# Kernel optimization log

Hardware: AMD Instinct MI355X
Metric: run time of the kernel (lower is better)

The kernel has to match this reference:

```python
import jax, jax.numpy as jnp
import numpy as np

# (in_ch, out_ch) per conv layer per SA stage (use_xyz adds +3 to first in-ch)
DIMS = {1: [(3, 64), (64, 64), (64, 128)],
        2: [(131, 128), (128, 128), (128, 256)],
        3: [(259, 256), (256, 512), (512, 1024)]}
B, N = 32, 4096


def setup_inputs() -> dict:
    key = jax.random.key(0)
    key, k = jax.random.split(key)
    inp = {"pointcloud": jax.random.uniform(k, (B, N, 3), jnp.float32)}
    for s in (1, 2, 3):
        for l, (ci, co) in enumerate(DIMS[s]):
            key, k1, k2, k3 = jax.random.split(key, 4)
            inp[f"w{s}{l}"] = jax.random.normal(k1, (ci, co), jnp.float32) * (1.0 / np.sqrt(ci))
            # eval-mode BatchNorm folded to per-channel scale g and bias b
            inp[f"g{s}{l}"] = 1.0 + 0.1 * jax.random.normal(k2, (co,), jnp.float32)
            inp[f"b{s}{l}"] = 0.1 * jax.random.normal(k3, (co,), jnp.float32)
    return inp


def fps(xyz, npoint):
    """Farthest point sampling. xyz: (B,N,3) -> idx (B,npoint) int32. First index is 0."""
    n = xyz.shape[1]
    def one(pts):
        def body(carry, _):
            dist, last = carry
            d = jnp.sum((pts - pts[last]) ** 2, axis=-1)
            dist = jnp.minimum(dist, d)
            nxt = jnp.argmax(dist).astype(jnp.int32)
            return (dist, nxt), nxt
        init = (jnp.full((n,), 1e10, pts.dtype), jnp.int32(0))
        _, idxs = jax.lax.scan(body, init, None, length=npoint - 1)
        return jnp.concatenate([jnp.zeros((1,), jnp.int32), idxs])
    return jax.vmap(one)(xyz)


def ball_query(xyz, centers, radius, nsample):
    """xyz (B,N,3), centers (B,S,3) -> idx (B,S,nsample): first nsample in-ball point
    indices, deficits padded with the first found index (matches CUDA ball_query)."""
    n = xyz.shape[1]
    d2 = jnp.sum((centers[:, :, None, :] - xyz[:, None, :, :]) ** 2, axis=-1)  # (B,S,N)
    keyv = jnp.where(d2 < radius * radius, jnp.arange(n)[None, None, :], n)
    sk = jnp.sort(keyv, axis=-1)[..., :nsample]  # ascending valid indices, pad = n
    first = sk[..., :1]
    idx = jnp.where(sk == n, first, sk)
    return jnp.clip(idx, 0, n - 1)


def gather(pts, idx):
    """pts (B,N,C), idx (B,...) -> (B,...,C)"""
    return jax.vmap(lambda p, i: p[i])(pts, idx)


def shared_mlp(x, params):
    """x (..., Cin); each layer: 1x1 conv (matmul) + folded-BN affine + ReLU."""
    for w, g, b in params:
        x = jax.nn.relu(jnp.einsum('...c,cd->...d', x, w) * g + b)
    return x


def sa_module(xyz, feat, npoint, radius, nsample, params):
    ctr_idx = fps(xyz, npoint)
    new_xyz = gather(xyz, ctr_idx)                        # (B,S,3)
    idx = ball_query(xyz, new_xyz, radius, nsample)       # (B,S,K)
    g_xyz = gather(xyz, idx) - new_xyz[:, :, None, :]     # (B,S,K,3) centered
    grouped = g_xyz if feat is None else jnp.concatenate([g_xyz, gather(feat, idx)], axis=-1)
    h = shared_mlp(grouped, params)                       # (B,S,K,Cout)
    return new_xyz, jnp.max(h, axis=2)                    # max-pool over neighbors


def reference(pointcloud, w10, g10, b10, w11, g11, b11, w12, g12, b12,
              w20, g20, b20, w21, g21, b21, w22, g22, b22,
              w30, g30, b30, w31, g31, b31, w32, g32, b32):
    p1 = [(w10, g10, b10), (w11, g11, b11), (w12, g12, b12)]
    p2 = [(w20, g20, b20), (w21, g21, b21), (w22, g22, b22)]
    p3 = [(w30, g30, b30), (w31, g31, b31), (w32, g32, b32)]
    xyz = pointcloud[..., :3]
    xyz, feat = sa_module(xyz, None, 512, 0.2, 64, p1)
    xyz, feat = sa_module(xyz, feat, 128, 0.4, 64, p2)
    # group-all SA: one group containing all points, xyz NOT centered
    grouped = jnp.concatenate([xyz, feat], axis=-1)[:, None]  # (B,1,S,259)
    h = shared_mlp(grouped, p3)                                # (B,1,S,1024)
    return jnp.max(h, axis=2)[:, 0]                            # (B,1024)
```

## Files before the change

### kernel.cpp

```cpp
#include <hip/hip_runtime.h>
#include <math.h>

#define NTH 256

using short8 = __attribute__((ext_vector_type(8))) short;
using f32x4  = __attribute__((ext_vector_type(4))) float;

__device__ __forceinline__ unsigned short f2bf(float x) {
    unsigned u = __float_as_uint(x);
    u += 0x7fff + ((u >> 16) & 1);
    return (unsigned short)(u >> 16);
}
__device__ __forceinline__ float bf2f(unsigned short h) {
    return __uint_as_float(((unsigned)h) << 16);
}

template<int CTRL>
__device__ __forceinline__ unsigned long long dppmax(unsigned long long k) {
    unsigned lo = (unsigned)k, hi = (unsigned)(k >> 32);
    unsigned plo = (unsigned)__builtin_amdgcn_update_dpp(0, (int)lo, CTRL, 0xF, 0xF, true);
    unsigned phi = (unsigned)__builtin_amdgcn_update_dpp(0, (int)hi, CTRL, 0xF, 0xF, true);
    unsigned long long p = ((unsigned long long)phi << 32) | plo;
    return p > k ? p : k;
}

template<int N, int NPOINT, int NTHR, int NPC, bool INIT, bool SPILL>
__device__ __forceinline__ void fps_body(
    const float* __restrict__ xyz, float* __restrict__ out_xyz, int b, int it0,
    float* __restrict__ pts , float* __restrict__ ctr ,
    unsigned long long* __restrict__ wkey ,
    float* __restrict__ sdist, int* __restrict__ slast)
{
    constexpr int PT = N / NTHR;
    constexpr int NW = NTHR / 64;
    const int tid  = threadIdx.x;
    const int lane = tid & 63;
    const int w    = tid >> 6;
    const float* src = xyz + (size_t)b * N * 3;

    __builtin_amdgcn_s_setprio(1);

    for (int e = tid; e < N * 3; e += NTHR) pts[e] = src[e];

    float px[PT], py[PT], pz[PT], dist[PT];
    unsigned klo[PT];
#pragma unroll
    for (int j = 0; j < PT; ++j) {
        int i = j * NTHR + tid;
        px[j] = src[i * 3 + 0]; py[j] = src[i * 3 + 1]; pz[j] = src[i * 3 + 2];
        klo[j] = ~(unsigned)i;
        dist[j] = 1e10f;
    }
    int last = 0;
    if constexpr (!INIT) {
        const float* sd = sdist + (size_t)b * N;
#pragma unroll
        for (int j = 0; j < PT; ++j) dist[j] = sd[j * NTHR + tid];
        last = slast[b];
    } else {
        if (tid == 0) { ctr[0] = src[0]; ctr[1] = src[1]; ctr[2] = src[2]; }
    }
    __syncthreads();

    constexpr int CBEG = INIT ? 1 : 0;
    for (int c = CBEG; c < NPC; ++c) {
        const float lx = pts[last * 3 + 0];
        const float ly = pts[last * 3 + 1];
        const float lz = pts[last * 3 + 2];
        unsigned long long best = 0ull;
#pragma unroll
        for (int j = 0; j < PT; ++j) {
            float dx = px[j] - lx, dy = py[j] - ly, dz = pz[j] - lz;
            float d = __fadd_rn(__fadd_rn(__fmul_rn(dx, dx), __fmul_rn(dy, dy)),
                                __fmul_rn(dz, dz));
            float nd = fminf(dist[j], d);
            dist[j] = nd;
            unsigned long long key =
                ((unsigned long long)__float_as_uint(nd) << 32) | (unsigned long long)klo[j];
            best = (key > best) ? key : best;
        }
        best = dppmax<0xB1>(best);
        best = dppmax<0x4E>(best);
        best = dppmax<0x141>(best);
        best = dppmax<0x140>(best);
        best = dppmax<0x142>(best);
        best = dppmax<0x143>(best);
        const int p = (c & 1) * NW;
        if (lane == 63) wkey[p + w] = best;
        __syncthreads();
        unsigned long long K0[NW];
#pragma unroll
        for (int v = 0; v < NW; ++v) K0[v] = wkey[p + v];
#pragma unroll
        for (int st = NW / 2; st > 0; st >>= 1)
#pragma unroll
            for (int v = 0; v < st; ++v) K0[v] = (K0[v + st] > K0[v]) ? K0[v + st] : K0[v];
        last = (int)(~(unsigned)K0[0]);
        if (tid == 0) {
            ctr[c * 3 + 0] = pts[last * 3 + 0];
            ctr[c * 3 + 1] = pts[last * 3 + 1];
            ctr[c * 3 + 2] = pts[last * 3 + 2];
        }
    }
    __syncthreads();
    if constexpr (SPILL) {
        float* sd = sdist + (size_t)b * N;
#pragma unroll
        for (int j = 0; j < PT; ++j) sd[j * NTHR + tid] = dist[j];
        if (tid == 0) slast[b] = last;
    }
    float* dst = out_xyz + ((size_t)b * NPOINT + (it0 - CBEG)) * 3;
    for (int e = tid; e < NPC * 3; e += NTHR) dst[e] = ctr[e];
    __builtin_amdgcn_s_setprio(0);
}

#define PREP_TOT 813056
__device__ __forceinline__ void prep_body(
    int gid, int stride,
    const float* __restrict__ w0, const float* __restrict__ w1, const float* __restrict__ w2,
    const float* __restrict__ w3, const float* __restrict__ w4, const float* __restrict__ w5,
    const float* __restrict__ w6, const float* __restrict__ w7, const float* __restrict__ w8,
    unsigned short* __restrict__ outw)
{
    const int K_[9]    = {3, 64, 64, 131, 128, 128, 259, 256, 512};
    const int N_[9]    = {64, 64, 128, 128, 128, 256, 256, 512, 1024};
    const int E_[9]    = {2048, 4096, 8192, 20480, 16384, 32768, 73728, 131072, 524288};
    const int base_[9] = {0, 4096, 12288, 28672, 69632, 102400, 167936, 315392, 577536};
    const int PCF_[9]  = {0, 0, 0, 128, 0, 0, 256, 0, 0};
    const float* W_[9] = {w0, w1, w2, w3, w4, w5, w6, w7, w8};
    for (; gid < PREP_TOT; gid += stride) {
        int i = 0, t = gid;
        while (t >= E_[i]) { t -= E_[i]; ++i; }
        const int Nn = N_[i];
        const int k8 = t / (Nn * 8);
        const int rem = t - k8 * Nn * 8;
        const int col = rem >> 3, j = rem & 7;
        const int k = k8 * 8 + j;
        float v = 0.f;
        if (k < K_[i]) {
            int ks = k;
            const int pcf = PCF_[i];
            if (pcf > 0) ks = (k < pcf) ? (k + 3) : (k - pcf);
            v = W_[i][(size_t)ks * Nn + col];
        }
        unsigned short hi = f2bf(v);
        unsigned short lo = f2bf(v - bf2f(hi));
        outw[base_[i] + t] = hi;
        outw[base_[i] + E_[i] + t] = lo;
    }
}

template<int K, int NSUB, int NOFF, int NFULL, int RTILES, int SX, int SY, bool FINAL>
__device__ __forceinline__ void mfma_layer(
    const unsigned short* __restrict__ whi, const unsigned short* __restrict__ wlo,
    const float* __restrict__ gm, const float* __restrict__ bt,
    const unsigned short* __restrict__ Xhi, const unsigned short* __restrict__ Xlo,
    unsigned short* __restrict__ Yhi, unsigned short* __restrict__ Ylo,
    float* outp, int tid)
{
    constexpr int KP  = (K + 31) & ~31;
    constexpr int KC  = KP / 32;
    constexpr int NTW = NSUB / 64;
    static_assert(NSUB % 64 == 0, "col split");
    const int w = tid >> 6, lane = tid & 63;
    const int lr = lane & 15, lg = lane >> 4;
    const int colbase = NOFF + w * (NSUB / 4);

    f32x4 acc[RTILES][NTW];
#pragma unroll
    for (int m = 0; m < RTILES; ++m)
#pragma unroll
        for (int t = 0; t < NTW; ++t) acc[m][t] = f32x4{0.f, 0.f, 0.f, 0.f};

    const unsigned short* xh0 = Xhi + lr * SX + lg * 8;
    const unsigned short* xl0 = Xlo + lr * SX + lg * 8;

    for (int kc = 0; kc < KC; ++kc) {
        const size_t krow = (size_t)(kc * 4 + lg) * NFULL * 8;
        short8 bh[NTW], bl[NTW];
#pragma unroll
        for (int t = 0; t < NTW; ++t) {
            const int col = colbase + t * 16 + lr;
            bh[t] = *reinterpret_cast<const short8*>(whi + krow + (size_t)col * 8);
            bl[t] = *reinterpret_cast<const short8*>(wlo + krow + (size_t)col * 8);
        }
#pragma unroll
        for (int m = 0; m < RTILES; ++m) {
            short8 ah = *reinterpret_cast<const short8*>(xh0 + m * 16 * SX + kc * 32);
            short8 al = *reinterpret_cast<const short8*>(xl0 + m * 16 * SX + kc * 32);
#pragma unroll
            for (int t = 0; t < NTW; ++t) {
                acc[m][t] = __builtin_amdgcn_mfma_f32_16x16x32_bf16(ah, bh[t], acc[m][t], 0, 0, 0);
                acc[m][t] = __builtin_amdgcn_mfma_f32_16x16x32_bf16(ah, bl[t], acc[m][t], 0, 0, 0);
                acc[m][t] = __builtin_amdgcn_mfma_f32_16x16x32_bf16(al, bh[t], acc[m][t], 0, 0, 0);
            }
        }
    }
#pragma unroll
    for (int t = 0; t < NTW; ++t) {
        const int col = colbase + t * 16 + lr;
        const float gv = gm[col], bv = bt[col];
        if constexpr (FINAL) {
            float mx = 0.f;
#pragma unroll
            for (int m = 0; m < RTILES; ++m)
#pragma unroll
                for (int r = 0; r < 4; ++r)
                    mx = fmaxf(mx, fmaxf(fmaf(acc[m][t][r], gv, bv), 0.f));
            mx = fmaxf(mx, __shfl_xor(mx, 16));
            mx = fmaxf(mx, __shfl_xor(mx, 32));
            if (lg == 0)
                atomicMax(reinterpret_cast<int*>(outp) + col, __float_as_int(mx));
        } else {
#pragma unroll
            for (int m = 0; m < RTILES; ++m)
#pragma unroll
                for (int r = 0; r < 4; ++r) {
                    float v = fmaxf(fmaf(acc[m][t][r], gv, bv), 0.f);
                    unsigned short hi = f2bf(v);
                    unsigned short lo = f2bf(v - bf2f(hi));
                    const int row = m * 16 + lg * 4 + r;
                    Yhi[row * SY + col] = hi;
                    Ylo[row * SY + col] = lo;
                }
        }
    }
}

template<int CF, int C0, int C1, int C2, int R>
struct SaCfg {
    static constexpr int CIN = 3 + CF;
    static constexpr int KP0 = (CIN + 31) & ~31;
    static constexpr int SX = KP0 + 8, SY1 = C0 + 8, SY2 = C1 + 8;
    static constexpr int RT = R / 16;
    static constexpr int OFF_Y1 = 0;
    static constexpr int OFF_X = 2 * R * SY1;
    static constexpr int XSZ = 2 * R * SX, Y2SZ = 2 * R * SY2;
    static constexpr int TOT = OFF_X + (XSZ > Y2SZ ? XSZ : Y2SZ);
    static constexpr int BYTES = TOT * 2 + 264 * 4;
};

template<int CF, int C0, int C1, int C2, int R>
__device__ __forceinline__ void sa_body(
    unsigned short* __restrict__ sm, int* __restrict__ bqm,
    int b, int cs, int S, int half,
    const float* __restrict__ src_xyz, const float* __restrict__ src_feat,
    const float* __restrict__ centers,
    const unsigned short* __restrict__ w0h, const unsigned short* __restrict__ w0l,
    const unsigned short* __restrict__ w1h, const unsigned short* __restrict__ w1l,
    const unsigned short* __restrict__ w2h, const unsigned short* __restrict__ w2l,
    const float* __restrict__ g0, const float* __restrict__ b0,
    const float* __restrict__ g1, const float* __restrict__ b1,
    const float* __restrict__ g2, const float* __restrict__ b2,
    float* __restrict__ out_feat, int N, float r2)
{
    using C = SaCfg<CF, C0, C1, C2, R>;
    constexpr int TPR = NTH / R;
    const int tid  = threadIdx.x;
    const int lane = tid & 63;
    const int w    = tid >> 6;
    const int bs   = b * S + cs;

    const float cx = centers[(size_t)bs * 3 + 0];
    const float cy = centers[(size_t)bs * 3 + 1];
    const float cz = centers[(size_t)bs * 3 + 2];

    {
        const int seg = N >> 2;
        const float* px = src_xyz + (size_t)b * N * 3;
        int count = 0, first = -1;
        const int bend = (w + 1) * seg;
        for (int base = w * seg; base < bend && count < 64; base += 64) {
            int i = base + lane;
            float dx = px[i * 3 + 0] - cx, dy = px[i * 3 + 1] - cy, dz = px[i * 3 + 2] - cz;
            float d2 = __fadd_rn(__fadd_rn(__fmul_rn(dx, dx), __fmul_rn(dy, dy)),
                                 __fmul_rn(dz, dz));
            bool inb = d2 < r2;
            unsigned long long m = __ballot(inb);
            if (first < 0 && m) first = base + (__ffsll(m) - 1);
            if (inb) {
                int pos = count + (int)__popcll(m & ((1ull << lane) - 1ull));
                if (pos < 64) bqm[w * 64 + pos] = i;
            }
            count += (int)__popcll(m);
        }
        if (lane == 0) {
            bqm[256 + w] = count > 64 ? 64 : count;
            bqm[260 + w] = first;
        }
    }
    __syncthreads();

    unsigned short* Xhi = sm + C::OFF_X;    unsigned short* Xlo = Xhi + R * C::SX;
    unsigned short* Y1h = sm + C::OFF_Y1;   unsigned short* Y1l = Y1h + R * C::SY1;
    unsigned short* Y2h = sm + C::OFF_X;    unsigned short* Y2l = Y2h + R * C::SY2;

    {
        const int r = tid / TPR, s = tid % TPR;
        int pid;
        {
            const int cA = bqm[256 + 0], cB = bqm[256 + 1], cC = bqm[256 + 2], cD = bqm[256 + 3];
            const int tot = cA + cB + cC + cD;
            int t = half * R + r;
            if (t < tot) {
                int ww = 0;
                if (t >= cA) { t -= cA; ww = 1;
                    if (t >= cB) { t -= cB; ww = 2;
                        if (t >= cC) { t -= cC; ww = 3; } } }
                pid = bqm[ww * 64 + t];
            } else {
                const int fA = bqm[260 + 0], fB = bqm[260 + 1], fC = bqm[260 + 2], fD = bqm[260 + 3];
                pid = fA >= 0 ? fA : (fB >= 0 ? fB : (fC >= 0 ? fC : (fD >= 0 ? fD : (N - 1))));
            }
        }
        unsigned short* xh = Xhi + r * C::SX;
        unsigned short* xl = Xlo + r * C::SX;
        if constexpr (CF > 0) {
            constexpr int CPT = CF / TPR;
            const float* frow = src_feat + ((size_t)b * N + pid) * CF + s * CPT;
#pragma unroll
            for (int q = 0; q < CPT / 4; ++q) {
                float4 v4 = *reinterpret_cast<const float4*>(frow + q * 4);
                ushort4 h, l;
                h.x = f2bf(v4.x); l.x = f2bf(v4.x - bf2f(h.x));
                h.y = f2bf(v4.y); l.y = f2bf(v4.y - bf2f(h.y));
                h.z = f2bf(v4.z); l.z = f2bf(v4.z - bf2f(h.z));
                h.w = f2bf(v4.w); l.w = f2bf(v4.w - bf2f(h.w));
                *reinterpret_cast<ushort4*>(xh + s * CPT + q * 4) = h;
                *reinterpret_cast<ushort4*>(xl + s * CPT + q * 4) = l;
            }
        }
        if (s < 3) {
            float p = src_xyz[((size_t)b * N + pid) * 3 + s]
                      - (s == 0 ? cx : (s == 1 ? cy : cz));
            unsigned short hi = f2bf(p), lo = f2bf(p - bf2f(hi));
            xh[CF + s] = hi; xl[CF + s] = lo;
        }
        constexpr int PADPER = (C::KP0 - C::CIN + TPR - 1) / TPR;
#pragma unroll
        for (int q = 0; q < PADPER; ++q) {
            int c = C::CIN + s * PADPER + q;
            if (c < C::KP0) { xh[c] = 0; xl[c] = 0; }
        }
    }
    __syncthreads();
    mfma_layer<C::CIN, C0, 0, C0, C::RT, C::SX, C::SY1, false>(
        w0h, w0l, g0, b0, Xhi, Xlo, Y1h, Y1l, nullptr, tid);
    __syncthreads();
    mfma_layer<C0, C1, 0, C1, C::RT, C::SY1, C::SY2, false>(
        w1h, w1l, g1, b1, Y1h, Y1l, Y2h, Y2l, nullptr, tid);
    __syncthreads();
    mfma_layer<C1, C2, 0, C2, C::RT, C::SY2, 0, true>(
        w2h, w2l, g2, b2, Y2h, Y2l, nullptr, nullptr,
        out_feat + (size_t)bs * C2, tid);
}

template<int N1>
__global__ __launch_bounds__(NTH) void k_fps1a_prep(
    const float* __restrict__ pc, float* __restrict__ nxyz1,
    const float* __restrict__ w0, const float* __restrict__ w1, const float* __restrict__ w2,
    const float* __restrict__ w3, const float* __restrict__ w4, const float* __restrict__ w5,
    const float* __restrict__ w6, const float* __restrict__ w7, const float* __restrict__ w8,
    unsigned short* __restrict__ outw,
    float* __restrict__ sdist, int* __restrict__ slast, int nfps)
{
    __shared__ float pts[N1 * 3];
    __shared__ float ctr[256 * 3];
    __shared__ unsigned long long wkey[2 * (NTH / 64)];
    if ((int)blockIdx.x < nfps) {
        fps_body<N1, 512, NTH, 256, true, true>(pc, nxyz1, blockIdx.x, 1,
                                                pts, ctr, wkey, sdist, slast);
    } else {
        prep_body((blockIdx.x - nfps) * NTH + threadIdx.x,
                  (gridDim.x - nfps) * NTH,
                  w0, w1, w2, w3, w4, w5, w6, w7, w8, outw);
    }
}

__global__ __launch_bounds__(NTH) void k_fps1b_sa1h1(
    const float* __restrict__ pc, float* __restrict__ nxyz1,
    float* __restrict__ sdist, int* __restrict__ slast,
    const unsigned short* __restrict__ w0h, const unsigned short* __restrict__ w0l,
    const unsigned short* __restrict__ w1h, const unsigned short* __restrict__ w1l,
    const unsigned short* __restrict__ w2h, const unsigned short* __restrict__ w2l,
    const float* __restrict__ g0, const float* __restrict__ b0,
    const float* __restrict__ g1, const float* __restrict__ b1,
    const float* __restrict__ g2, const float* __restrict__ b2,
    float* __restrict__ feat1, float r2)
{
    constexpr int FPSB = 4096 * 3 * 4 + 256 * 3 * 4 + 2 * (NTH / 64) * 8;
    constexpr int SAB  = SaCfg<0, 64, 64, 128, 64>::BYTES;
    constexpr int BYTES = FPSB > SAB ? FPSB : SAB;
    __shared__ __align__(16) char raw[BYTES];
    if ((int)blockIdx.x < 32) {
        float* pts = (float*)raw;
        float* ctr = (float*)(raw + 4096 * 3 * 4);
        unsigned long long* wkey = (unsigned long long*)(raw + 4096 * 3 * 4 + 256 * 3 * 4);
        fps_body<4096, 512, NTH, 256, false, false>(pc, nxyz1, blockIdx.x, 256,
                                                    pts, ctr, wkey, sdist, slast);
    } else {
        const int blk = blockIdx.x - 32;
        const int b = blk >> 8, cs = blk & 255;
        unsigned short* sm = (unsigned short*)raw;
        int* bqm = (int*)(raw + SaCfg<0, 64, 64, 128, 64>::TOT * 2);
        sa_body<0, 64, 64, 128, 64>(sm, bqm, b, cs, 512, 0,
                                    pc, nullptr, nxyz1,
                                    w0h, w0l, w1h, w1l, w2h, w2l,
                                    g0, b0, g1, b1, g2, b2, feat1, 4096, r2);
    }
}

__global__ __launch_bounds__(NTH) void k_fps2_sa1h2(
    const float* __restrict__ pc, const float* __restrict__ nxyz1_c,
    float* __restrict__ nxyz1, float* __restrict__ nxyz2,
    const unsigned short* __restrict__ w0h, const unsigned short* __restrict__ w0l,
    const unsigned short* __restrict__ w1h, const unsigned short* __restrict__ w1l,
    const unsigned short* __restrict__ w2h, const unsigned short* __restrict__ w2l,
    const float* __restrict__ g0, const float* __restrict__ b0,
    const float* __restrict__ g1, const float* __restrict__ b1,
    const float* __restrict__ g2, const float* __restrict__ b2,
    float* __restrict__ feat1, float r2)
{
    constexpr int FPSB = 512 * 3 * 4 + 128 * 3 * 4 + 2 * (NTH / 64) * 8;
    constexpr int SAB  = SaCfg<0, 64, 64, 128, 64>::BYTES;
    constexpr int BYTES = FPSB > SAB ? FPSB : SAB;
    __shared__ __align__(16) char raw[BYTES];
    if ((int)blockIdx.x < 32) {
        float* pts = (float*)raw;
        float* ctr = (float*)(raw + 512 * 3 * 4);
        unsigned long long* wkey = (unsigned long long*)(raw + 512 * 3 * 4 + 128 * 3 * 4);
        fps_body<512, 128, NTH, 128, true, false>(nxyz1, nxyz2, blockIdx.x, 1,
                                                  pts, ctr, wkey, nullptr, nullptr);
    } else {
        const int blk = blockIdx.x - 32;
        const int b = blk >> 8, cs = 256 + (blk & 255);
        unsigned short* sm = (unsigned short*)raw;
        int* bqm = (int*)(raw + SaCfg<0, 64, 64, 128, 64>::TOT * 2);
        sa_body<0, 64, 64, 128, 64>(sm, bqm, b, cs, 512, 0,
                                    pc, nullptr, nxyz1_c,
                                    w0h, w0l, w1h, w1l, w2h, w2l,
                                    g0, b0, g1, b1, g2, b2, feat1, 4096, r2);
    }
}

__global__ __launch_bounds__(NTH) void k_sa2(
    const float* __restrict__ nxyz1, const float* __restrict__ feat1,
    const float* __restrict__ nxyz2,
    const unsigned short* __restrict__ w0h, const unsigned short* __restrict__ w0l,
    const unsigned short* __restrict__ w1h, const unsigned short* __restrict__ w1l,
    const unsigned short* __restrict__ w2h, const unsigned short* __restrict__ w2l,
    const float* __restrict__ g0, const float* __restrict__ b0,
    const float* __restrict__ g1, const float* __restrict__ b1,
    const float* __restrict__ g2, const float* __restrict__ b2,
    float* __restrict__ feat2, float r2)
{
    using C = SaCfg<128, 128, 128, 256, 32>;
    __shared__ __align__(16) char raw[C::BYTES];
    const int half = blockIdx.x & 1;
    const int cb   = blockIdx.x >> 1;
    const int b = cb >> 7, cs = cb & 127;
    unsigned short* sm = (unsigned short*)raw;
    int* bqm = (int*)(raw + C::TOT * 2);
    sa_body<128, 128, 128, 256, 32>(sm, bqm, b, cs, 128, half,
                                    nxyz1, feat1, nxyz2,
                                    w0h, w0l, w1h, w1l, w2h, w2l,
                                    g0, b0, g1, b1, g2, b2, feat2, 512, r2);
}

template<int CF, int C0, int C1, int C2>
__global__ __launch_bounds__(NTH) void head_mfma(
    const float* __restrict__ xyz, const float* __restrict__ feat,
    const unsigned short* __restrict__ w0h, const unsigned short* __restrict__ w0l,
    const unsigned short* __restrict__ w1h, const unsigned short* __restrict__ w1l,
    const unsigned short* __restrict__ w2h, const unsigned short* __restrict__ w2l,
    const float* __restrict__ g0, const float* __restrict__ b0,
    const float* __restrict__ g1, const float* __restrict__ b1,
    const float* __restrict__ g2, const float* __restrict__ b2,
    float* __restrict__ out, int Np)
{
    constexpr int R = 16;
    constexpr int CIN = 3 + CF;
    constexpr int KP0 = (CIN + 31) & ~31;
    constexpr int SX = KP0 + 8, SY1 = C0 + 8, SY2 = C1 + 8;
    constexpr int OFF_Y1 = 0;
    constexpr int OFF_X  = 2 * R * SY1;
    constexpr int XSZ = 2 * R * SX, Y2SZ = 2 * R * SY2;
    constexpr int TOT = OFF_X + (XSZ > Y2SZ ? XSZ : Y2SZ);
    __shared__ __align__(16) unsigned short sm[TOT];
    constexpr int TPR = NTH / R;

    const int tid = threadIdx.x;
    const int chunks = Np / R;
    const int b  = blockIdx.x / chunks;
    const int r0 = (blockIdx.x % chunks) * R;

    unsigned short* Xhi = sm + OFF_X;   unsigned short* Xlo = Xhi + R * SX;
    unsigned short* Y1h = sm + OFF_Y1;  unsigned short* Y1l = Y1h + R * SY1;
    unsigned short* Y2h = sm + OFF_X;   unsigned short* Y2l = Y2h + R * SY2;

    {
        const int r = tid / TPR, s = tid % TPR;
        const int row = r0 + r;
        unsigned short* xh = Xhi + r * SX;
        unsigned short* xl = Xlo + r * SX;
        constexpr int CPT = CF / TPR;
        const float* frow = feat + ((size_t)b * Np + row) * CF + s * CPT;
#pragma unroll
        for (int q = 0; q < CPT / 4; ++q) {
            float4 v4 = *reinterpret_cast<const float4*>(frow + q * 4);
            ushort4 h, l;
            h.x = f2bf(v4.x); l.x = f2bf(v4.x - bf2f(h.x));
            h.y = f2bf(v4.y); l.y = f2bf(v4.y - bf2f(h.y));
            h.z = f2bf(v4.z); l.z = f2bf(v4.z - bf2f(h.z));
            h.w = f2bf(v4.w); l.w = f2bf(v4.w - bf2f(h.w));
            *reinterpret_cast<ushort4*>(xh + s * CPT + q * 4) = h;
            *reinterpret_cast<ushort4*>(xl + s * CPT + q * 4) = l;
        }
        if (s < 3) {
            float p = xyz[((size_t)b * Np + row) * 3 + s];
            unsigned short hi = f2bf(p), lo = f2bf(p - bf2f(hi));
            xh[CF + s] = hi; xl[CF + s] = lo;
        }
        constexpr int PADPER = (KP0 - CIN + TPR - 1) / TPR;
#pragma unroll
        for (int q = 0; q < PADPER; ++q) {
            int c = CIN + s * PADPER + q;
            if (c < KP0) { xh[c] = 0; xl[c] = 0; }
        }
    }
    __syncthreads();
    mfma_layer<CIN, C0, 0, C0, 1, SX, SY1, false>(w0h, w0l, g0, b0, Xhi, Xlo, Y1h, Y1l, nullptr, tid);
    __syncthreads();
    mfma_layer<C0, C1, 0, C1, 1, SY1, SY2, false>(w1h, w1l, g1, b1, Y1h, Y1l, Y2h, Y2l, nullptr, tid);
    __syncthreads();
    float* op = out + (size_t)b * C2;
    mfma_layer<C1, C2 / 2, 0,      C2, 1, SY2, 0, true>(w2h, w2l, g2, b2, Y2h, Y2l, nullptr, nullptr, op, tid);
    mfma_layer<C1, C2 / 2, C2 / 2, C2, 1, SY2, 0, true>(w2h, w2l, g2, b2, Y2h, Y2l, nullptr, nullptr, op, tid);
}

extern "C" void kernel_launch(void* const* d_in, const int* in_sizes, int n_in,
                              void* d_out, int out_size, void* d_ws, size_t ws_size,
                              hipStream_t stream)
{
    (void)in_sizes; (void)n_in; (void)ws_size;
    const int B = 32;
    const float* pc = (const float*)d_in[0];
    const float* W[27];
    for (int i = 0; i < 27; ++i) W[i] = (const float*)d_in[1 + i];
    float* out = (float*)d_out;

    char* ws = (char*)d_ws;
    size_t off = 0;
    auto take = [&](size_t bytes) {
        void* p = ws + off;
        off += (bytes + 255) & ~(size_t)255;
        return p;
    };
    float* nxyz1 = (float*)take((size_t)B * 512 * 3 * 4);
    float* feat1 = (float*)take((size_t)B * 512 * 128 * 4);
    float* nxyz2 = (float*)take((size_t)B * 128 * 3 * 4);
    float* feat2 = (float*)take((size_t)B * 128 * 256 * 4);
    unsigned short* wf = (unsigned short*)take((size_t)1626112 * 2);
    float* sdist = (float*)take((size_t)B * 4096 * 4);
    int*   slast = (int*)take((size_t)B * 4);

    const int E_[9]    = {2048, 4096, 8192, 20480, 16384, 32768, 73728, 131072, 524288};
    const int base_[9] = {0, 4096, 12288, 28672, 69632, 102400, 167936, 315392, 577536};
    const unsigned short* wh[9]; const unsigned short* wl[9];
    for (int i = 0; i < 9; ++i) { wh[i] = wf + base_[i]; wl[i] = wf + base_[i] + E_[i]; }

    hipMemsetAsync(feat1, 0, (size_t)B * 512 * 128 * 4, stream);
    hipMemsetAsync(feat2, 0, (size_t)B * 128 * 256 * 4, stream);
    hipMemsetAsync(d_out, 0, (size_t)out_size * 4, stream);

    const float r2_1 = (float)(0.2 * 0.2);
    const float r2_2 = (float)(0.4 * 0.4);

    k_fps1a_prep<4096><<<32 + 512, NTH, 0, stream>>>(
        pc, nxyz1,
        W[0], W[3], W[6], W[9], W[12], W[15], W[18], W[21], W[24],
        wf, sdist, slast, 32);

    k_fps1b_sa1h1<<<32 + B * 256, NTH, 0, stream>>>(
        pc, nxyz1, sdist, slast,
        wh[0], wl[0], wh[1], wl[1], wh[2], wl[2],
        W[1], W[2], W[4], W[5], W[7], W[8],
        feat1, r2_1);

    k_fps2_sa1h2<<<32 + B * 256, NTH, 0, stream>>>(
        pc, nxyz1, nxyz1, nxyz2,
        wh[0], wl[0], wh[1], wl[1], wh[2], wl[2],
        W[1], W[2], W[4], W[5], W[7], W[8],
        feat1, r2_1);

    k_sa2<<<B * 128 * 2, NTH, 0, stream>>>(
        nxyz1, feat1, nxyz2,
        wh[3], wl[3], wh[4], wl[4], wh[5], wl[5],
        W[10], W[11], W[13], W[14], W[16], W[17],
        feat2, r2_2);

    head_mfma<256, 256, 512, 1024><<<B * 8, NTH, 0, stream>>>(
        nxyz2, feat2,
        wh[6], wl[6], wh[7], wl[7], wh[8], wl[8],
        W[19], W[20], W[22], W[23], W[25], W[26],
        out, 128);
}
```

Before: 612.4 us.

## Fold output zeroing into prep kernel and run stage-2 FPS after stage-1 FPS

Three hipMemsetAsync calls are replaced by zeroing blocks appended to the first prep/FPS kernel, which removes separate memset launches. The second-stage FPS now runs inside the same blocks that finish the first-stage FPS, right after it completes. The second SA1 half is therefore a plain SA kernel. This shortens the serial FPS chain across kernel boundaries, but stage-2 FPS now overlaps with the SA1 first-half blocks instead of the second-half ones.

```diff
diff --git a/kernel.cpp b/kernel.cpp
--- a/kernel.cpp
+++ b/kernel.cpp
@@ -362,7 +362,9 @@
     const float* __restrict__ w3, const float* __restrict__ w4, const float* __restrict__ w5,
     const float* __restrict__ w6, const float* __restrict__ w7, const float* __restrict__ w8,
     unsigned short* __restrict__ outw,
-    float* __restrict__ sdist, int* __restrict__ slast, int nfps)
+    float* __restrict__ sdist, int* __restrict__ slast,
+    float4* __restrict__ z1, int n1, float4* __restrict__ z2, int n2,
+    float4* __restrict__ z3, int n3, int nfps, int nprep)
 {
     __shared__ float pts[N1 * 3];
     __shared__ float ctr[256 * 3];
@@ -370,15 +372,21 @@
     if ((int)blockIdx.x < nfps) {
         fps_body<N1, 512, NTH, 256, true, true>(pc, nxyz1, blockIdx.x, 1,
                                                 pts, ctr, wkey, sdist, slast);
+    } else if ((int)blockIdx.x < nfps + nprep) {
+        prep_body((blockIdx.x - nfps) * NTH + threadIdx.x, nprep * NTH,
+                  w0, w1, w2, w3, w4, w5, w6, w7, w8, outw);
     } else {
-        prep_body((blockIdx.x - nfps) * NTH + threadIdx.x,
-                  (gridDim.x - nfps) * NTH,
-                  w0, w1, w2, w3, w4, w5, w6, w7, w8, outw);
-    }
-}
-
-__global__ __launch_bounds__(NTH) void k_fps1b_sa1h1(
-    const float* __restrict__ pc, float* __restrict__ nxyz1,
+        const int zid = (blockIdx.x - nfps - nprep) * NTH + threadIdx.x;
+        const int zs  = (gridDim.x - nfps - nprep) * NTH;
+        const float4 zv = make_float4(0.f, 0.f, 0.f, 0.f);
+        for (int i = zid; i < n1; i += zs) z1[i] = zv;
+        for (int i = zid; i < n2; i += zs) z2[i] = zv;
+        for (int i = zid; i < n3; i += zs) z3[i] = zv;
+    }
+}
+
+__global__ __launch_bounds__(NTH) void k_fps1b2_sa1h1(
+    const float* __restrict__ pc, float* __restrict__ nxyz1, float* __restrict__ nxyz2,
     float* __restrict__ sdist, int* __restrict__ slast,
     const unsigned short* __restrict__ w0h, const unsigned short* __restrict__ w0l,
     const unsigned short* __restrict__ w1h, const unsigned short* __restrict__ w1l,
@@ -393,11 +401,21 @@
     constexpr int BYTES = FPSB > SAB ? FPSB : SAB;
     __shared__ __align__(16) char raw[BYTES];
     if ((int)blockIdx.x < 32) {
-        float* pts = (float*)raw;
-        float* ctr = (float*)(raw + 4096 * 3 * 4);
-        unsigned long long* wkey = (unsigned long long*)(raw + 4096 * 3 * 4 + 256 * 3 * 4);
-        fps_body<4096, 512, NTH, 256, false, false>(pc, nxyz1, blockIdx.x, 256,
-                                                    pts, ctr, wkey, sdist, slast);
+        {
+            float* pts = (float*)raw;
+            float* ctr = (float*)(raw + 4096 * 3 * 4);
+            unsigned long long* wkey = (unsigned long long*)(raw + 4096 * 3 * 4 + 256 * 3 * 4);
+            fps_body<4096, 512, NTH, 256, false, false>(pc, nxyz1, blockIdx.x, 256,
+                                                        pts, ctr, wkey, sdist, slast);
+        }
+        __syncthreads();
+        {
+            float* pts = (float*)raw;
+            float* ctr = (float*)(raw + 512 * 3 * 4);
+            unsigned long long* wkey = (unsigned long long*)(raw + 512 * 3 * 4 + 128 * 3 * 4);
+            fps_body<512, 128, NTH, 128, true, false>(nxyz1, nxyz2, blockIdx.x, 1,
+                                                      pts, ctr, wkey, nullptr, nullptr);
+        }
     } else {
         const int blk = blockIdx.x - 32;
         const int b = blk >> 8, cs = blk & 255;
@@ -410,9 +428,8 @@
     }
 }
 
-__global__ __launch_bounds__(NTH) void k_fps2_sa1h2(
-    const float* __restrict__ pc, const float* __restrict__ nxyz1_c,
-    float* __restrict__ nxyz1, float* __restrict__ nxyz2,
+__global__ __launch_bounds__(NTH) void k_sa1h2(
+    const float* __restrict__ pc, const float* __restrict__ nxyz1,
     const unsigned short* __restrict__ w0h, const unsigned short* __restrict__ w0l,
     const unsigned short* __restrict__ w1h, const unsigned short* __restrict__ w1l,
     const unsigned short* __restrict__ w2h, const unsigned short* __restrict__ w2l,
@@ -421,26 +438,15 @@
     const float* __restrict__ g2, const float* __restrict__ b2,
     float* __restrict__ feat1, float r2)
 {
-    constexpr int FPSB = 512 * 3 * 4 + 128 * 3 * 4 + 2 * (NTH / 64) * 8;
-    constexpr int SAB  = SaCfg<0, 64, 64, 128, 64>::BYTES;
-    constexpr int BYTES = FPSB > SAB ? FPSB : SAB;
-    __shared__ __align__(16) char raw[BYTES];
-    if ((int)blockIdx.x < 32) {
-        float* pts = (float*)raw;
-        float* ctr = (float*)(raw + 512 * 3 * 4);
-        unsigned long long* wkey = (unsigned long long*)(raw + 512 * 3 * 4 + 128 * 3 * 4);
-        fps_body<512, 128, NTH, 128, true, false>(nxyz1, nxyz2, blockIdx.x, 1,
-                                                  pts, ctr, wkey, nullptr, nullptr);
-    } else {
-        const int blk = blockIdx.x - 32;
-        const int b = blk >> 8, cs = 256 + (blk & 255);
-        unsigned short* sm = (unsigned short*)raw;
-        int* bqm = (int*)(raw + SaCfg<0, 64, 64, 128, 64>::TOT * 2);
-        sa_body<0, 64, 64, 128, 64>(sm, bqm, b, cs, 512, 0,
-                                    pc, nullptr, nxyz1_c,
-                                    w0h, w0l, w1h, w1l, w2h, w2l,
-                                    g0, b0, g1, b1, g2, b2, feat1, 4096, r2);
-    }
+    using C = SaCfg<0, 64, 64, 128, 64>;
+    __shared__ __align__(16) char raw[C::BYTES];
+    const int b = blockIdx.x >> 8, cs = 256 + (blockIdx.x & 255);
+    unsigned short* sm = (unsigned short*)raw;
+    int* bqm = (int*)(raw + C::TOT * 2);
+    sa_body<0, 64, 64, 128, 64>(sm, bqm, b, cs, 512, 0,
+                                pc, nullptr, nxyz1,
+                                w0h, w0l, w1h, w1l, w2h, w2l,
+                                g0, b0, g1, b1, g2, b2, feat1, 4096, r2);
 }
 
 __global__ __launch_bounds__(NTH) void k_sa2(
@@ -569,26 +575,26 @@
     const unsigned short* wh[9]; const unsigned short* wl[9];
     for (int i = 0; i < 9; ++i) { wh[i] = wf + base_[i]; wl[i] = wf + base_[i] + E_[i]; }
 
-    hipMemsetAsync(feat1, 0, (size_t)B * 512 * 128 * 4, stream);
-    hipMemsetAsync(feat2, 0, (size_t)B * 128 * 256 * 4, stream);
-    hipMemsetAsync(d_out, 0, (size_t)out_size * 4, stream);
-
     const float r2_1 = (float)(0.2 * 0.2);
     const float r2_2 = (float)(0.4 * 0.4);
 
-    k_fps1a_prep<4096><<<32 + 512, NTH, 0, stream>>>(
+    k_fps1a_prep<4096><<<32 + 512 + 64, NTH, 0, stream>>>(
         pc, nxyz1,
         W[0], W[3], W[6], W[9], W[12], W[15], W[18], W[21], W[24],
-        wf, sdist, slast, 32);
-
-    k_fps1b_sa1h1<<<32 + B * 256, NTH, 0, stream>>>(
-        pc, nxyz1, sdist, slast,
+        wf, sdist, slast,
+        (float4*)feat1, B * 512 * 128 / 4,
+        (float4*)feat2, B * 128 * 256 / 4,
+        (float4*)out,   out_size / 4,
+        32, 512);
+
+    k_fps1b2_sa1h1<<<32 + B * 256, NTH, 0, stream>>>(
+        pc, nxyz1, nxyz2, sdist, slast,
         wh[0], wl[0], wh[1], wl[1], wh[2], wl[2],
         W[1], W[2], W[4], W[5], W[7], W[8],
         feat1, r2_1);
 
-    k_fps2_sa1h2<<<32 + B * 256, NTH, 0, stream>>>(
-        pc, nxyz1, nxyz1, nxyz2,
+    k_sa1h2<<<B * 256, NTH, 0, stream>>>(
+        pc, nxyz1,
         wh[0], wl[0], wh[1], wl[1], wh[2], wl[2],
         W[1], W[2], W[4], W[5], W[7], W[8],
         feat1, r2_1);
```

After: 649.6 us. 1.06x slower.
